# Kernel tuning notes

Hardware: AMD Instinct MI355X
Metric: run time of the kernel (lower is better)

Reference implementation:

```python
import jax, jax.numpy as jnp
import numpy as np

T, B, H, V, L = 1024, 16, 1024, 100, 3


def setup_inputs() -> dict:
    key = jax.random.key(0)
    k_x, k_e, k_w, k_b = jax.random.split(key, 4)
    x = jax.random.randint(k_x, (T, B), 0, V)                      # [T, B] token ids
    emb = jax.random.normal(k_e, (V, H), dtype=jnp.float32) * 0.1  # embedding table
    # per-layer Linear(H, 3H): stacked weights/biases (all layers have in=out=H)
    W = jax.random.normal(k_w, (L, H, 3 * H), dtype=jnp.float32) * (1.0 / np.sqrt(H))
    b = jax.random.normal(k_b, (L, 3 * H), dtype=jnp.float32) * 0.01
    return {"x": x, "emb": emb, "W": W, "b": b}


def _qrnn_layer(h, W_l, b_l):
    # h: [T, B, H] -> gates [T, B, 3H]
    g = jnp.einsum("tbh,hk->tbk", h, W_l) + b_l
    z, f, o = jnp.split(g, 3, axis=-1)
    z = jnp.tanh(z)
    f = jax.nn.sigmoid(f)
    o = jax.nn.sigmoid(o)

    def step(c, zf):
        z_t, f_t = zf
        c = f_t * z_t + (1.0 - f_t) * c  # forget-mult recurrence
        return c, c

    c0 = jnp.zeros(h.shape[1:], dtype=h.dtype)  # hidden init is None -> zeros
    _, C = jax.lax.scan(step, c0, (z, f))       # C: [T, B, H]
    return o * C


def reference(x, emb, W, b):
    h = emb[x]  # [T, B, H]
    for l in range(L):
        h = _qrnn_layer(h, W[l], b[l])
    return h[:-1]  # drop last timestep, [T-1, B, H]
```

## Files before the change

kernel.cpp:

```cpp
#include <hip/hip_runtime.h>
#include <hip/hip_bf16.h>

#define T_DIM 1024
#define B_DIM 16
#define H_DIM 1024
#define L_DIM 3
#define M_DIM (T_DIM * B_DIM)
#define N_DIM (3 * H_DIM)
#define K_DIM H_DIM
#define NC 32
#define CS 32

typedef __bf16 bf16x8 __attribute__((ext_vector_type(8)));
typedef __bf16 bf16x4 __attribute__((ext_vector_type(4)));
typedef _Float16 half4 __attribute__((ext_vector_type(4)));
typedef float f32x4 __attribute__((ext_vector_type(4)));

__device__ __forceinline__ __bf16 f2bf(float f) {
    return (__bf16)__float2bfloat16(f);
}

__device__ __forceinline__ void async_cp16(const void* g, void* lds) {
    __builtin_amdgcn_global_load_lds(
        (__attribute__((address_space(1))) void*)g,
        (__attribute__((address_space(3))) void*)lds, 16, 0, 0);
}

__global__ void transpose_w(const float* __restrict__ W, __bf16* __restrict__ Wt) {
    __shared__ __bf16 tile[32][33];
    const int l = blockIdx.z;
    const int k0 = blockIdx.x * 32, n0 = blockIdx.y * 32;
    const int tx = threadIdx.x & 31, ty = threadIdx.x >> 5;
    const float* Wl = W + (size_t)l * K_DIM * N_DIM;
    __bf16* Wtl = Wt + (size_t)l * N_DIM * K_DIM;
#pragma unroll
    for (int q = 0; q < 4; q++) {
        int k = ty + q * 8;
        tile[k][tx] = f2bf(Wl[(size_t)(k0 + k) * N_DIM + n0 + tx]);
    }
    __syncthreads();
#pragma unroll
    for (int q = 0; q < 4; q++) {
        int n = ty + q * 8;
        Wtl[(size_t)(n0 + n) * K_DIM + k0 + tx] = tile[tx][n];
    }
}

__global__ void embed_kernel(const int* __restrict__ x,
                             const float4* __restrict__ emb,
                             __bf16* __restrict__ h) {
    int i = blockIdx.x * 256 + threadIdx.x;
    int row = i >> 8;
    int j = i & 255;
    int idx = x[row];
    float4 v = emb[(size_t)idx * 256 + j];
    __bf16* dst = h + (size_t)row * H_DIM + j * 4;
    dst[0] = f2bf(v.x); dst[1] = f2bf(v.y); dst[2] = f2bf(v.z); dst[3] = f2bf(v.w);
}

__global__ __launch_bounds__(256, 2) void gemm_gates(
    const __bf16* __restrict__ A,
    const __bf16* __restrict__ Wt,
    const float* __restrict__ bias,
    _Float16* __restrict__ Gz, _Float16* __restrict__ Gf, _Float16* __restrict__ Go) {
    __shared__ __align__(16) __bf16 As[128 * 32];
    __shared__ __align__(16) __bf16 Bs[128 * 32];

    const int tid = threadIdx.x;
    const int wid = tid >> 6, lane = tid & 63;
    const int bm = blockIdx.x, bn = blockIdx.y;
    const int waveM = wid >> 1, waveN = wid & 1;
    const int lm = lane & 15, kg = lane >> 4;

    const int r0 = tid >> 2;
    const int cc = (((tid & 3) ^ ((r0 >> 1) & 3))) * 8;
    const int r1 = r0 + 64;
    const __bf16* Abase = A + (size_t)(bm * 128) * K_DIM;
    const __bf16* Bbase = Wt + (size_t)(bn * 128) * K_DIM;
    __bf16* ldsA0 = As + (size_t)wid * 512;
    __bf16* ldsA1 = As + (size_t)wid * 512 + 2048;
    __bf16* ldsB0 = Bs + (size_t)wid * 512;
    __bf16* ldsB1 = Bs + (size_t)wid * 512 + 2048;

    const int csw = (kg ^ ((lm >> 1) & 3)) * 8;

    f32x4 acc[4][4] = {};

    for (int k0 = 0; k0 < K_DIM; k0 += 32) {
        async_cp16(Abase + (size_t)r0 * K_DIM + k0 + cc, ldsA0);
        async_cp16(Abase + (size_t)r1 * K_DIM + k0 + cc, ldsA1);
        async_cp16(Bbase + (size_t)r0 * K_DIM + k0 + cc, ldsB0);
        async_cp16(Bbase + (size_t)r1 * K_DIM + k0 + cc, ldsB1);
        __syncthreads();

        bf16x8 af[4], bf[4];
#pragma unroll
        for (int i = 0; i < 4; i++)
            af[i] = *(const bf16x8*)(As + (waveM * 64 + i * 16 + lm) * 32 + csw);
#pragma unroll
        for (int j = 0; j < 4; j++)
            bf[j] = *(const bf16x8*)(Bs + (waveN * 64 + j * 16 + lm) * 32 + csw);
#pragma unroll
        for (int i = 0; i < 4; i++)
#pragma unroll
            for (int j = 0; j < 4; j++)
                acc[i][j] = __builtin_amdgcn_mfma_f32_16x16x32_bf16(af[i], bf[j], acc[i][j], 0, 0, 0);
        __syncthreads();
    }

    const int plane = bn >> 3;
    _Float16* __restrict__ P = (plane == 0) ? Gz : (plane == 1) ? Gf : Go;
#pragma unroll
    for (int i = 0; i < 4; i++) {
#pragma unroll
        for (int j = 0; j < 4; j++) {
            int ncol = bn * 128 + waveN * 64 + j * 16 + lm;
            int col = ncol & 1023;
            float bv = bias[ncol];
#pragma unroll
            for (int r = 0; r < 4; r++) {
                int mrow = bm * 128 + waveM * 64 + i * 16 + kg * 4 + r;
                float g = acc[i][j][r] + bv;
                float val;
                if (plane == 0) {
                    float e = __expf(-2.0f * fabsf(g));
                    val = copysignf((1.0f - e) / (1.0f + e), g);
                } else {
                    val = 1.0f / (1.0f + __expf(-g));
                }
                P[(size_t)mrow * H_DIM + col] = (_Float16)val;
            }
        }
    }
}

__global__ void scan_pass1(const _Float16* __restrict__ Gz, const _Float16* __restrict__ Gf,
                           float* __restrict__ cA, float* __restrict__ cM) {
    int tid = blockIdx.x * 256 + threadIdx.x;
    int ci = tid >> 12;
    int b = (tid >> 8) & 15;
    int hg = tid & 255;
    size_t base = ((size_t)(ci * CS) * B_DIM + b) * H_DIM + hg * 4;
    f32x4 Aacc = {0.f, 0.f, 0.f, 0.f};
    f32x4 Macc = {1.f, 1.f, 1.f, 1.f};
#pragma unroll 8
    for (int s = 0; s < CS; s++) {
        half4 z = *(const half4*)(Gz + base);
        half4 f = *(const half4*)(Gf + base);
#pragma unroll
        for (int k = 0; k < 4; k++) {
            float fk = (float)f[k], zk = (float)z[k];
            Aacc[k] = fk * zk + (1.f - fk) * Aacc[k];
            Macc[k] = (1.f - fk) * Macc[k];
        }
        base += (size_t)B_DIM * H_DIM;
    }
    size_t idx = (size_t)ci * 16384 + 4 * (size_t)(tid & 4095);
    *(f32x4*)(cA + idx) = Aacc;
    *(f32x4*)(cM + idx) = Macc;
}

__global__ void scan_pass2(const float* __restrict__ cA, const float* __restrict__ cM,
                           float* __restrict__ cIn) {
    int ch = blockIdx.x * 256 + threadIdx.x;
    float c = 0.f;
#pragma unroll
    for (int ci = 0; ci < NC; ci++) {
        cIn[ci * 16384 + ch] = c;
        c = cA[ci * 16384 + ch] + cM[ci * 16384 + ch] * c;
    }
}

__global__ void scan_pass3(const _Float16* __restrict__ Gz, const _Float16* __restrict__ Gf,
                           const _Float16* __restrict__ Go, const float* __restrict__ cIn,
                           __bf16* __restrict__ hdst, float* __restrict__ fdst,
                           int is_last) {
    int tid = blockIdx.x * 256 + threadIdx.x;
    int ci = tid >> 12;
    int b = (tid >> 8) & 15;
    int hg = tid & 255;
    size_t base = ((size_t)(ci * CS) * B_DIM + b) * H_DIM + hg * 4;
    f32x4 c = *(const f32x4*)(cIn + (size_t)ci * 16384 + 4 * (size_t)(tid & 4095));
#pragma unroll 4
    for (int s = 0; s < CS; s++) {
        int t = ci * CS + s;
        half4 z = *(const half4*)(Gz + base);
        half4 f = *(const half4*)(Gf + base);
        half4 o = *(const half4*)(Go + base);
        f32x4 val;
#pragma unroll
        for (int k = 0; k < 4; k++) {
            float fk = (float)f[k];
            c[k] = fk * (float)z[k] + (1.f - fk) * c[k];
            val[k] = (float)o[k] * c[k];
        }
        if (is_last) {
            if (t < T_DIM - 1)
                *(f32x4*)(fdst + base) = val;
        } else {
            bf16x4 hv;
#pragma unroll
            for (int k = 0; k < 4; k++) hv[k] = f2bf(val[k]);
            *(bf16x4*)(hdst + base) = hv;
        }
        base += (size_t)B_DIM * H_DIM;
    }
}

extern "C" void kernel_launch(void* const* d_in, const int* in_sizes, int n_in,
                              void* d_out, int out_size, void* d_ws, size_t ws_size,
                              hipStream_t stream) {
    const int* x = (const int*)d_in[0];
    const float* emb = (const float*)d_in[1];
    const float* W = (const float*)d_in[2];
    const float* b = (const float*)d_in[3];
    float* out = (float*)d_out;

    char* ws = (char*)d_ws;
    size_t need = (size_t)L_DIM * N_DIM * K_DIM * 2
                + (size_t)M_DIM * H_DIM * 2
                + 3ull * M_DIM * H_DIM * 2
                + 3ull * NC * 16384 * 4;
    if (ws_size < need) return;

    __bf16* Wt = (__bf16*)ws;     ws += (size_t)L_DIM * N_DIM * K_DIM * 2;
    __bf16* hbuf = (__bf16*)ws;   ws += (size_t)M_DIM * H_DIM * 2;
    _Float16* Gz = (_Float16*)ws; ws += (size_t)M_DIM * H_DIM * 2;
    _Float16* Gf = (_Float16*)ws; ws += (size_t)M_DIM * H_DIM * 2;
    _Float16* Go = (_Float16*)ws; ws += (size_t)M_DIM * H_DIM * 2;
    float* cA = (float*)ws;       ws += (size_t)NC * 16384 * 4;
    float* cM = (float*)ws;       ws += (size_t)NC * 16384 * 4;
    float* cIn = (float*)ws;

    transpose_w<<<dim3(K_DIM / 32, N_DIM / 32, L_DIM), 256, 0, stream>>>(W, Wt);
    embed_kernel<<<(M_DIM * H_DIM / 4) / 256, 256, 0, stream>>>(x, (const float4*)emb, hbuf);

    for (int l = 0; l < L_DIM; l++) {
        gemm_gates<<<dim3(M_DIM / 128, N_DIM / 128), 256, 0, stream>>>(
            hbuf, Wt + (size_t)l * N_DIM * K_DIM, b + (size_t)l * N_DIM, Gz, Gf, Go);
        scan_pass1<<<131072 / 256, 256, 0, stream>>>(Gz, Gf, cA, cM);
        scan_pass2<<<16384 / 256, 256, 0, stream>>>(cA, cM, cIn);
        int last = (l == L_DIM - 1);
        scan_pass3<<<131072 / 256, 256, 0, stream>>>(Gz, Gf, Go, cIn, hbuf, out, last);
    }
}
```

Measured before the change: 639.7 us.

## Double GEMM K-tile, merge prep kernels, shorten scan chunks, use fast reciprocals

The GEMM K tile per barrier goes from 32 to 64 with a new XOR swizzle, halving the number of sync/load rounds per output tile. The weight transpose and embedding kernels are merged into one launch. The scan uses 64 chunks of 16 steps instead of 32 of 32, giving more parallel threads, with full unrolling and launch bounds. The gate activations use hardware reciprocal approximations in place of divisions. Together these raise LDS use per block, trade some precision in the activations, and add a little work to the sequential chunk-combine pass.

```diff
diff --git a/kernel.cpp b/kernel.cpp
--- a/kernel.cpp
+++ b/kernel.cpp
@@ -8,8 +8,8 @@
 #define M_DIM (T_DIM * B_DIM)
 #define N_DIM (3 * H_DIM)
 #define K_DIM H_DIM
-#define NC 32
-#define CS 32
+#define NC 64
+#define CS 16
 
 typedef __bf16 bf16x8 __attribute__((ext_vector_type(8)));
 typedef __bf16 bf16x4 __attribute__((ext_vector_type(4)));
@@ -26,36 +26,39 @@
         (__attribute__((address_space(3))) void*)lds, 16, 0, 0);
 }
 
-__global__ void transpose_w(const float* __restrict__ W, __bf16* __restrict__ Wt) {
-    __shared__ __bf16 tile[32][33];
-    const int l = blockIdx.z;
-    const int k0 = blockIdx.x * 32, n0 = blockIdx.y * 32;
-    const int tx = threadIdx.x & 31, ty = threadIdx.x >> 5;
-    const float* Wl = W + (size_t)l * K_DIM * N_DIM;
-    __bf16* Wtl = Wt + (size_t)l * N_DIM * K_DIM;
-#pragma unroll
-    for (int q = 0; q < 4; q++) {
-        int k = ty + q * 8;
-        tile[k][tx] = f2bf(Wl[(size_t)(k0 + k) * N_DIM + n0 + tx]);
-    }
-    __syncthreads();
-#pragma unroll
-    for (int q = 0; q < 4; q++) {
-        int n = ty + q * 8;
-        Wtl[(size_t)(n0 + n) * K_DIM + k0 + tx] = tile[tx][n];
-    }
-}
-
-__global__ void embed_kernel(const int* __restrict__ x,
-                             const float4* __restrict__ emb,
-                             __bf16* __restrict__ h) {
-    int i = blockIdx.x * 256 + threadIdx.x;
-    int row = i >> 8;
-    int j = i & 255;
-    int idx = x[row];
-    float4 v = emb[(size_t)idx * 256 + j];
-    __bf16* dst = h + (size_t)row * H_DIM + j * 4;
-    dst[0] = f2bf(v.x); dst[1] = f2bf(v.y); dst[2] = f2bf(v.z); dst[3] = f2bf(v.w);
+#define TW_BLOCKS (32 * 96 * 3)
+__global__ void prep_kernel(const float* __restrict__ W, __bf16* __restrict__ Wt,
+                            const int* __restrict__ x, const float4* __restrict__ emb,
+                            __bf16* __restrict__ h) {
+    if (blockIdx.x < TW_BLOCKS) {
+        __shared__ __bf16 tile[32][33];
+        const int blk = blockIdx.x;
+        const int l = blk / 3072;
+        const int r2 = blk % 3072;
+        const int n0 = (r2 / 32) * 32, k0 = (r2 % 32) * 32;
+        const int tx = threadIdx.x & 31, ty = threadIdx.x >> 5;
+        const float* Wl = W + (size_t)l * K_DIM * N_DIM;
+        __bf16* Wtl = Wt + (size_t)l * N_DIM * K_DIM;
+#pragma unroll
+        for (int q = 0; q < 4; q++) {
+            int k = ty + q * 8;
+            tile[k][tx] = f2bf(Wl[(size_t)(k0 + k) * N_DIM + n0 + tx]);
+        }
+        __syncthreads();
+#pragma unroll
+        for (int q = 0; q < 4; q++) {
+            int n = ty + q * 8;
+            Wtl[(size_t)(n0 + n) * K_DIM + k0 + tx] = tile[tx][n];
+        }
+    } else {
+        int i = (blockIdx.x - TW_BLOCKS) * 256 + threadIdx.x;
+        int row = i >> 8;
+        int j = i & 255;
+        int idx = x[row];
+        float4 v = emb[(size_t)idx * 256 + j];
+        __bf16* dst = h + (size_t)row * H_DIM + j * 4;
+        dst[0] = f2bf(v.x); dst[1] = f2bf(v.y); dst[2] = f2bf(v.z); dst[3] = f2bf(v.w);
+    }
 }
 
 __global__ __launch_bounds__(256, 2) void gemm_gates(
@@ -63,8 +66,8 @@
     const __bf16* __restrict__ Wt,
     const float* __restrict__ bias,
     _Float16* __restrict__ Gz, _Float16* __restrict__ Gf, _Float16* __restrict__ Go) {
-    __shared__ __align__(16) __bf16 As[128 * 32];
-    __shared__ __align__(16) __bf16 Bs[128 * 32];
+    __shared__ __align__(16) __bf16 As[128 * 64];
+    __shared__ __align__(16) __bf16 Bs[128 * 64];
 
     const int tid = threadIdx.x;
     const int wid = tid >> 6, lane = tid & 63;
@@ -72,39 +75,46 @@
     const int waveM = wid >> 1, waveN = wid & 1;
     const int lm = lane & 15, kg = lane >> 4;
 
-    const int r0 = tid >> 2;
-    const int cc = (((tid & 3) ^ ((r0 >> 1) & 3))) * 8;
-    const int r1 = r0 + 64;
+    int roff[4], loff[4];
+#pragma unroll
+    for (int q = 0; q < 4; q++) {
+        int cell = q * 256 + tid;
+        int r = cell >> 3, s = cell & 7;
+        int g = s ^ (r & 7);
+        roff[q] = r * K_DIM + g * 8;
+        loff[q] = (q * 256 + wid * 64) * 8;
+    }
+
     const __bf16* Abase = A + (size_t)(bm * 128) * K_DIM;
     const __bf16* Bbase = Wt + (size_t)(bn * 128) * K_DIM;
-    __bf16* ldsA0 = As + (size_t)wid * 512;
-    __bf16* ldsA1 = As + (size_t)wid * 512 + 2048;
-    __bf16* ldsB0 = Bs + (size_t)wid * 512;
-    __bf16* ldsB1 = Bs + (size_t)wid * 512 + 2048;
-
-    const int csw = (kg ^ ((lm >> 1) & 3)) * 8;
 
     f32x4 acc[4][4] = {};
 
-    for (int k0 = 0; k0 < K_DIM; k0 += 32) {
-        async_cp16(Abase + (size_t)r0 * K_DIM + k0 + cc, ldsA0);
-        async_cp16(Abase + (size_t)r1 * K_DIM + k0 + cc, ldsA1);
-        async_cp16(Bbase + (size_t)r0 * K_DIM + k0 + cc, ldsB0);
-        async_cp16(Bbase + (size_t)r1 * K_DIM + k0 + cc, ldsB1);
+    for (int k0 = 0; k0 < K_DIM; k0 += 64) {
+#pragma unroll
+        for (int q = 0; q < 4; q++)
+            async_cp16(Abase + k0 + roff[q], As + loff[q]);
+#pragma unroll
+        for (int q = 0; q < 4; q++)
+            async_cp16(Bbase + k0 + roff[q], Bs + loff[q]);
         __syncthreads();
 
-        bf16x8 af[4], bf[4];
-#pragma unroll
-        for (int i = 0; i < 4; i++)
-            af[i] = *(const bf16x8*)(As + (waveM * 64 + i * 16 + lm) * 32 + csw);
-#pragma unroll
-        for (int j = 0; j < 4; j++)
-            bf[j] = *(const bf16x8*)(Bs + (waveN * 64 + j * 16 + lm) * 32 + csw);
-#pragma unroll
-        for (int i = 0; i < 4; i++)
+#pragma unroll
+        for (int h = 0; h < 2; h++) {
+            const int cs = ((h * 4 + kg) ^ (lane & 7)) * 8;
+            bf16x8 af[4], bf[4];
+#pragma unroll
+            for (int i = 0; i < 4; i++)
+                af[i] = *(const bf16x8*)(As + (waveM * 64 + i * 16 + lm) * 64 + cs);
 #pragma unroll
             for (int j = 0; j < 4; j++)
-                acc[i][j] = __builtin_amdgcn_mfma_f32_16x16x32_bf16(af[i], bf[j], acc[i][j], 0, 0, 0);
+                bf[j] = *(const bf16x8*)(Bs + (waveN * 64 + j * 16 + lm) * 64 + cs);
+#pragma unroll
+            for (int i = 0; i < 4; i++)
+#pragma unroll
+                for (int j = 0; j < 4; j++)
+                    acc[i][j] = __builtin_amdgcn_mfma_f32_16x16x32_bf16(af[i], bf[j], acc[i][j], 0, 0, 0);
+        }
         __syncthreads();
     }
 
@@ -124,9 +134,11 @@
                 float val;
                 if (plane == 0) {
                     float e = __expf(-2.0f * fabsf(g));
-                    val = copysignf((1.0f - e) / (1.0f + e), g);
+                    float rc = __builtin_amdgcn_rcpf(1.0f + e);
+                    val = copysignf(fmaf(-2.0f * e, rc, 1.0f), g);
                 } else {
-                    val = 1.0f / (1.0f + __expf(-g));
+                    float e = __expf(-g);
+                    val = __builtin_amdgcn_rcpf(1.0f + e);
                 }
                 P[(size_t)mrow * H_DIM + col] = (_Float16)val;
             }
@@ -134,16 +146,16 @@
     }
 }
 
-__global__ void scan_pass1(const _Float16* __restrict__ Gz, const _Float16* __restrict__ Gf,
-                           float* __restrict__ cA, float* __restrict__ cM) {
+__global__ __launch_bounds__(256, 8) void scan_pass1(
+    const _Float16* __restrict__ Gz, const _Float16* __restrict__ Gf,
+    float* __restrict__ cA, float* __restrict__ cM) {
     int tid = blockIdx.x * 256 + threadIdx.x;
     int ci = tid >> 12;
-    int b = (tid >> 8) & 15;
-    int hg = tid & 255;
-    size_t base = ((size_t)(ci * CS) * B_DIM + b) * H_DIM + hg * 4;
+    int cg = tid & 4095;
+    size_t base = (size_t)(ci * CS) * 16384 + (size_t)cg * 4;
     f32x4 Aacc = {0.f, 0.f, 0.f, 0.f};
     f32x4 Macc = {1.f, 1.f, 1.f, 1.f};
-#pragma unroll 8
+#pragma unroll
     for (int s = 0; s < CS; s++) {
         half4 z = *(const half4*)(Gz + base);
         half4 f = *(const half4*)(Gf + base);
@@ -153,15 +165,16 @@
             Aacc[k] = fk * zk + (1.f - fk) * Aacc[k];
             Macc[k] = (1.f - fk) * Macc[k];
         }
-        base += (size_t)B_DIM * H_DIM;
-    }
-    size_t idx = (size_t)ci * 16384 + 4 * (size_t)(tid & 4095);
+        base += 16384;
+    }
+    size_t idx = (size_t)ci * 16384 + (size_t)cg * 4;
     *(f32x4*)(cA + idx) = Aacc;
     *(f32x4*)(cM + idx) = Macc;
 }
 
-__global__ void scan_pass2(const float* __restrict__ cA, const float* __restrict__ cM,
-                           float* __restrict__ cIn) {
+__global__ __launch_bounds__(256, 8) void scan_pass2(
+    const float* __restrict__ cA, const float* __restrict__ cM,
+    float* __restrict__ cIn) {
     int ch = blockIdx.x * 256 + threadIdx.x;
     float c = 0.f;
 #pragma unroll
@@ -171,17 +184,16 @@
     }
 }
 
-__global__ void scan_pass3(const _Float16* __restrict__ Gz, const _Float16* __restrict__ Gf,
-                           const _Float16* __restrict__ Go, const float* __restrict__ cIn,
-                           __bf16* __restrict__ hdst, float* __restrict__ fdst,
-                           int is_last) {
+__global__ __launch_bounds__(256, 8) void scan_pass3(
+    const _Float16* __restrict__ Gz, const _Float16* __restrict__ Gf,
+    const _Float16* __restrict__ Go, const float* __restrict__ cIn,
+    __bf16* __restrict__ hdst, float* __restrict__ fdst, int is_last) {
     int tid = blockIdx.x * 256 + threadIdx.x;
     int ci = tid >> 12;
-    int b = (tid >> 8) & 15;
-    int hg = tid & 255;
-    size_t base = ((size_t)(ci * CS) * B_DIM + b) * H_DIM + hg * 4;
-    f32x4 c = *(const f32x4*)(cIn + (size_t)ci * 16384 + 4 * (size_t)(tid & 4095));
-#pragma unroll 4
+    int cg = tid & 4095;
+    size_t base = (size_t)(ci * CS) * 16384 + (size_t)cg * 4;
+    f32x4 c = *(const f32x4*)(cIn + (size_t)ci * 16384 + (size_t)cg * 4);
+#pragma unroll
     for (int s = 0; s < CS; s++) {
         int t = ci * CS + s;
         half4 z = *(const half4*)(Gz + base);
@@ -203,7 +215,7 @@
             for (int k = 0; k < 4; k++) hv[k] = f2bf(val[k]);
             *(bf16x4*)(hdst + base) = hv;
         }
-        base += (size_t)B_DIM * H_DIM;
+        base += 16384;
     }
 }
 
@@ -232,15 +244,14 @@
     float* cM = (float*)ws;       ws += (size_t)NC * 16384 * 4;
     float* cIn = (float*)ws;
 
-    transpose_w<<<dim3(K_DIM / 32, N_DIM / 32, L_DIM), 256, 0, stream>>>(W, Wt);
-    embed_kernel<<<(M_DIM * H_DIM / 4) / 256, 256, 0, stream>>>(x, (const float4*)emb, hbuf);
+    prep_kernel<<<TW_BLOCKS + 16384, 256, 0, stream>>>(W, Wt, x, (const float4*)emb, hbuf);
 
     for (int l = 0; l < L_DIM; l++) {
         gemm_gates<<<dim3(M_DIM / 128, N_DIM / 128), 256, 0, stream>>>(
             hbuf, Wt + (size_t)l * N_DIM * K_DIM, b + (size_t)l * N_DIM, Gz, Gf, Go);
-        scan_pass1<<<131072 / 256, 256, 0, stream>>>(Gz, Gf, cA, cM);
+        scan_pass1<<<(NC * 4096) / 256, 256, 0, stream>>>(Gz, Gf, cA, cM);
         scan_pass2<<<16384 / 256, 256, 0, stream>>>(cA, cM, cIn);
         int last = (l == L_DIM - 1);
-        scan_pass3<<<131072 / 256, 256, 0, stream>>>(Gz, Gf, Go, cIn, hbuf, out, last);
-    }
-}
+        scan_pass3<<<(NC * 4096) / 256, 256, 0, stream>>>(Gz, Gf, Go, cIn, hbuf, out, last);
+    }
+}
```

After: 559.5 us. -12.5%, faster.
